# Kernel optimization log

Hardware: AMD Instinct MI355X
Metric: run time of the kernel (lower is better)

The kernel has to match this reference:

```python
import jax, jax.numpy as jnp
import numpy as np

P1 = np.array([[1000.0, 0.0, 128.0, 64000.0],
               [0.0, 1000.0, 128.0, 64000.0],
               [0.0, 0.0, 1.0, 500.0]])
P2 = np.array([[-128.0, 0.0, 1000.0, 64000.0],
               [-128.0, 1000.0, 0.0, 64000.0],
               [-1.0, 0.0, 0.0, 500.0]])


def calculate_fundamental_matrix(P_src, P_dst):
    # l2 = F21 @ x1 : maps a point in P_src onto a line in P_dst
    C1 = -np.linalg.inv(P_src[:3, :3]) @ P_src[:3, 3]
    e = P_dst @ np.append(C1, 1.0)          # epipole of src camera center in dst view
    return np.cross(e, np.eye(3) * -1) @ P_dst @ np.linalg.pinv(P_src)


def setup_inputs() -> dict:
    key = jax.random.key(0)
    view1 = jax.random.normal(key, (8, 4, 256, 256), dtype=jnp.float32)
    F21 = calculate_fundamental_matrix(P1, P2).astype(np.float32)
    return {"view1": view1, "F": jnp.asarray(F21)}


def reference(view1, F):
    """Epipolar image translation: out(x2) = line integral of view1 along the
    epipolar line l1 = F^T @ x2 (bilinear sampling in v, unit steps in u,
    zero outside the image). Matches fume_torch_lib.translate semantics."""
    B, C, H, W = view1.shape
    dt = view1.dtype
    F = F.astype(dt)
    ys = jnp.arange(H, dtype=dt)[:, None]   # (H,1)
    xs = jnp.arange(W, dtype=dt)[None, :]   # (1,W)
    # line coefficients l = F^T @ [x, y, 1], per output pixel -> (H,W)
    a = F[0, 0] * xs + F[1, 0] * ys + F[2, 0]
    b = F[0, 1] * xs + F[1, 1] * ys + F[2, 1]
    c = F[0, 2] * xs + F[1, 2] * ys + F[2, 2]
    n = jnp.sqrt(a * a + b * b) + jnp.asarray(1e-12, dt)
    a, b, c = a / n, b / n, c / n
    ok = (jnp.abs(b) > 1e-6).astype(dt)                 # drop near-vertical lines
    b_safe = jnp.where(jnp.abs(b) > 1e-6, b, jnp.asarray(1.0, dt))

    def step(acc, u):
        uf = u.astype(dt)
        v = -(a * uf + c) / b_safe                      # (H,W) source row per out pixel
        v0 = jnp.floor(v)
        f = v - v0
        i0 = v0.astype(jnp.int32)
        i1 = i0 + 1
        m0 = ((i0 >= 0) & (i0 < H)).astype(dt)
        m1 = ((i1 >= 0) & (i1 < H)).astype(dt)
        col = jax.lax.dynamic_index_in_dim(view1, u, axis=3, keepdims=False)  # (B,C,H)
        s0 = col[:, :, jnp.clip(i0, 0, H - 1)]          # (B,C,H,W)
        s1 = col[:, :, jnp.clip(i1, 0, H - 1)]
        val = (s0 * (1.0 - f) * m0 + s1 * f * m1) * ok
        return acc + val, None

    out, _ = jax.lax.scan(step, jnp.zeros_like(view1), jnp.arange(W))
    return out
```

## Files before the change

### kernel.cpp

```cpp
#include <hip/hip_runtime.h>
#include <cstdint>

constexpr int Hh = 256, Ww = 256, BCc = 32;
constexpr int RBLK = 35;
constexpr int USTRIDE = RBLK * BCc * 8 * 2;

typedef _Float16 half2v  __attribute__((ext_vector_type(2)));
typedef _Float16 half8v  __attribute__((ext_vector_type(8)));
typedef __fp16   fp16x2  __attribute__((ext_vector_type(2)));
typedef float    float4v __attribute__((ext_vector_type(4)));
typedef uint32_t uint4v  __attribute__((ext_vector_type(4)));

static __device__ inline half2v pack2(float a, float b) {
    fp16x2 r = __builtin_amdgcn_cvt_pkrtz(a, b);
    return __builtin_bit_cast(half2v, r);
}

__global__ __launch_bounds__(256) void fume_zero(char* __restrict__ T4) {
    int id = blockIdx.x * 256 + threadIdx.x;
    int u, blk, ch;
    if (id < 257 * 3 * 32) {
        u = id / 96;
        int rem = id - u * 96;
        int bsel = rem >> 5;
        blk = (bsel == 0) ? 0 : (bsel == 1 ? 33 : 34);
        ch = rem & 31;
    } else if (id < 257 * 3 * 32 + 32 * 32) {
        int id2 = id - 257 * 3 * 32;
        u = 256; blk = 1 + (id2 >> 5); ch = id2 & 31;
    } else {
        return;
    }
    uint4v z = {0, 0, 0, 0};
    *(uint4v*)(T4 + (size_t)u * USTRIDE + blk * 512 + ch * 16) = z;
}

__global__ __launch_bounds__(256) void fume_pack(const float* __restrict__ in,
                                                 char* __restrict__ T4) {
    __shared__ float tile[32][65];
    const int t   = threadIdx.x;
    const int bid = blockIdx.x;
    const int chg = bid >> 5;
    const int r0  = ((bid >> 2) & 7) * 32;
    const int u0  = (bid & 3) * 64;

    for (int ci = 0; ci < 8; ++ci) {
        int ch = chg * 8 + ci;
#pragma unroll
        for (int it = 0; it < 8; ++it) {
            int idx = it * 256 + t;
            tile[idx >> 6][idx & 63] =
                in[ch * (Hh * Ww) + (r0 + (idx >> 6)) * Ww + u0 + (idx & 63)];
        }
        __syncthreads();
        int u_l = t >> 2, rs = (t & 3) * 8;
        uint32_t w[4];
#pragma unroll
        for (int j = 0; j < 4; ++j) {
            half2v p = pack2(tile[rs + 2 * j][u_l], tile[rs + 2 * j + 1][u_l]);
            __builtin_memcpy(&w[j], &p, 4);
        }
        int blk = ((r0 + rs) >> 3) + 1;
        uint4v val = {w[0], w[1], w[2], w[3]};
        *(uint4v*)(T4 + (size_t)(u0 + u_l) * USTRIDE + blk * 512 + ch * 16) = val;
        __syncthreads();
    }
}

__global__ __launch_bounds__(256, 8) void fume_mfma(const char* __restrict__ T4,
                                                    const float* __restrict__ Fm,
                                                    float* __restrict__ out) {
    __shared__ float red1[2][16][32];
    __shared__ float red2[2][16][32];
    const int t    = threadIdx.x;
    const int lane = t & 63;
    const int wv   = t >> 6;
    const int uh   = wv & 1;
    const int ly   = wv >> 1;
    const int px   = lane & 15;
    const int quad = lane >> 4;
    const int x0   = ((int)blockIdx.x & 15) * 16;
    const int y    = ((int)blockIdx.x >> 4) * 2 + ly;
    const int x    = x0 + px;

    float xf = (float)x, yf = (float)y;
    float a = Fm[0] * xf + Fm[3] * yf + Fm[6];
    float b = Fm[1] * xf + Fm[4] * yf + Fm[7];
    float c = Fm[2] * xf + Fm[5] * yf + Fm[8];
    float n = sqrtf(a * a + b * b) + 1e-12f;
    a /= n; b /= n; c /= n;

    float alpha, beta_i;
    int u_lo, u_hi;
    if (fabsf(b) > 1e-6f) {
        alpha  = -a / b;
        beta_i = -c / b + 8.f;
        u_lo = 0; u_hi = Ww - 1;
        if (fabsf(alpha) > 1e-12f) {
            float inv = 1.f / alpha;
            float t0 = (7.f - beta_i) * inv;
            float t1 = (264.f - beta_i) * inv;
            int lo = (int)floorf(fminf(t0, t1));
            int hi = (int)ceilf (fmaxf(t0, t1));
            u_lo = lo > 0 ? lo : 0;
            u_hi = hi < (Ww - 1) ? hi : (Ww - 1);
        } else if (beta_i <= 7.f || beta_i >= 264.f) {
            u_lo = 1 << 20; u_hi = -(1 << 20);
        }
    } else {
        alpha = 0.f; beta_i = 3.0e4f;
        u_lo = 1 << 20; u_hi = -(1 << 20);
    }

    float xA = (float)x0, xB = (float)(x0 + 15);
    float aA = Fm[0] * xA + Fm[3] * yf + Fm[6];
    float bA = Fm[1] * xA + Fm[4] * yf + Fm[7];
    float cA = Fm[2] * xA + Fm[5] * yf + Fm[8];
    float aB = Fm[0] * xB + Fm[3] * yf + Fm[6];
    float bB = Fm[1] * xB + Fm[4] * yf + Fm[7];
    float cB = Fm[2] * xB + Fm[5] * yf + Fm[8];
    float alA = -aA / bA, beA = -cA / bA + 8.f;
    float alB = -aB / bB, beB = -cB / bB + 8.f;

    int lo = u_lo, hi = u_hi;
#pragma unroll
    for (int off = 1; off < 64; off <<= 1) {
        int l2 = __shfl_xor(lo, off, 64);
        int h2 = __shfl_xor(hi, off, 64);
        lo = lo < l2 ? lo : l2;
        hi = hi > h2 ? hi : h2;
    }
    lo = __builtin_amdgcn_readfirstlane(lo);
    hi = __builtin_amdgcn_readfirstlane(hi);

    float4v acc0 = {0.f, 0.f, 0.f, 0.f};
    float4v acc1 = {0.f, 0.f, 0.f, 0.f};

    if (lo <= hi) {
        int len = hi - lo + 1;
        int h0  = (((len + 1) >> 1) + 1) & ~1;
        int us, nch;
        if (uh == 0) { us = lo;      nch = h0 >> 1; }
        else {
            int rem = len - h0;
            us = lo + h0;
            nch = rem > 0 ? ((rem + 1) >> 1) : 0;
        }

        float v   = fmaf(alpha, (float)(us + (quad >> 1)), beta_i);
        float a2  = 2.f * alpha;
        float vA0 = fmaf(alA, (float)us, beA);
        float vB0 = fmaf(alB, (float)us, beB);
        float aA2 = 2.f * alA, aB2 = 2.f * alB;
        float lane8 = (float)((quad & 1) * 8);
        const int lane_fix = (quad >> 1) * USTRIDE + (quad & 1) * 512 + px * 16;
        int ubase = us * USTRIDE;

        const half2v one2  = {(_Float16)1.f, (_Float16)1.f};
        const half2v zero2 = {(_Float16)0.f, (_Float16)0.f};

        for (int cc = 0; cc < nch; ++cc) {
            float mn = fminf(fminf(vA0, vA0 + alA), fminf(vB0, vB0 + alB));
            float Mf = floorf(fmaf(mn, 0.125f, -0.125f));
            Mf = fmaxf(0.f, fminf(Mf, 33.f));
            int soff = ubase + ((int)Mf << 9);
            soff = __builtin_amdgcn_readfirstlane(soff);

            uint4v b0 = *(const uint4v*)(T4 + soff + lane_fix);
            uint4v b1 = *(const uint4v*)(T4 + soff + lane_fix + 256);

            float vbl = fmaf(Mf, -8.f, v) - lane8;
            half2v vb2 = pack2(vbl, vbl);
            uint32_t aw[4];
#pragma unroll
            for (int j = 0; j < 4; ++j) {
                half2v cj = {(_Float16)(float)(2 * j),
                             (_Float16)(float)(2 * j + 1)};
                half2v d  = vb2 - cj;
                half2v ad = __builtin_elementwise_abs(d);
                half2v tj = __builtin_elementwise_max(one2 - ad, zero2);
                __builtin_memcpy(&aw[j], &tj, 4);
            }
            half8v A;
            __builtin_memcpy(&A, aw, 16);

            half8v B0 = __builtin_bit_cast(half8v, b0);
            half8v B1 = __builtin_bit_cast(half8v, b1);
            acc0 = __builtin_amdgcn_mfma_f32_16x16x32_f16(A, B0, acc0, 0, 0, 0);
            acc1 = __builtin_amdgcn_mfma_f32_16x16x32_f16(A, B1, acc1, 0, 0, 0);

            v += a2; vA0 += aA2; vB0 += aB2; ubase += 2 * USTRIDE;
        }
    }

    if (uh == 1) {
#pragma unroll
        for (int r = 0; r < 4; ++r) {
            int pm = quad * 4 + r;
            red1[ly][pm][(px + pm) & 31]      = acc0[r];
            red1[ly][pm][(px + 16 + pm) & 31] = acc1[r];
        }
    }
    __syncthreads();
    if (uh == 0) {
#pragma unroll
        for (int r = 0; r < 4; ++r) {
            int pm = quad * 4 + r;
            red2[ly][pm][(px + pm) & 31] =
                acc0[r] + red1[ly][pm][(px + pm) & 31];
            red2[ly][pm][(px + 16 + pm) & 31] =
                acc1[r] + red1[ly][pm][(px + 16 + pm) & 31];
        }
    }
    __syncthreads();
    {
        int ly2 = t >> 7, s = t & 127, pxs = s & 15, cg = s >> 4;
        int yy = ((int)blockIdx.x >> 4) * 2 + ly2;
#pragma unroll
        for (int j = 0; j < 4; ++j) {
            int ch = cg * 4 + j;
            float val = red2[ly2][pxs][(ch + pxs) & 31];
            out[(size_t)ch * (Hh * Ww) + yy * Ww + x0 + pxs] = val;
        }
    }
}

__global__ __launch_bounds__(256) void fume_fallback(const float* __restrict__ src,
                                                     const float* __restrict__ Fm,
                                                     float* __restrict__ out) {
    int g = blockIdx.x * 256 + threadIdx.x;
    int part = g & 3;
    int pix  = g >> 2;
    int x = pix & (Ww - 1);
    int y = pix >> 8;
    int ch0 = part * 8;
    float xf = (float)x, yf = (float)y;
    float a = Fm[0] * xf + Fm[3] * yf + Fm[6];
    float b = Fm[1] * xf + Fm[4] * yf + Fm[7];
    float c = Fm[2] * xf + Fm[5] * yf + Fm[8];
    float n = sqrtf(a * a + b * b) + 1e-12f;
    a /= n; b /= n; c /= n;
    float acc[8];
#pragma unroll
    for (int k = 0; k < 8; ++k) acc[k] = 0.f;
    if (fabsf(b) > 1e-6f) {
        float alpha = -a / b, beta = -c / b;
        for (int u = 0; u < Ww; ++u) {
            float v  = fmaf(alpha, (float)u, beta);
            float rf = floorf(v);
            float f  = v - rf;
            int   ri = (int)rf;
            float w0 = ((unsigned)ri       < (unsigned)Hh) ? (1.f - f) : 0.f;
            float w1 = ((unsigned)(ri + 1) < (unsigned)Hh) ? f         : 0.f;
            int r0 = ri < 0 ? 0 : (ri > Hh - 1 ? Hh - 1 : ri);
            int r1 = ri + 1 < 0 ? 0 : (ri + 1 > Hh - 1 ? Hh - 1 : ri + 1);
#pragma unroll
            for (int k = 0; k < 8; ++k) {
                float s0 = src[(size_t)(ch0 + k) * (Hh * Ww) + r0 * Ww + u];
                float s1 = src[(size_t)(ch0 + k) * (Hh * Ww) + r1 * Ww + u];
                acc[k] = fmaf(w0, s0, fmaf(w1, s1, acc[k]));
            }
        }
    }
#pragma unroll
    for (int k = 0; k < 8; ++k)
        out[(size_t)(ch0 + k) * (Hh * Ww) + pix] = acc[k];
}

extern "C" void kernel_launch(void* const* d_in, const int* in_sizes, int n_in,
                              void* d_out, int out_size, void* d_ws, size_t ws_size,
                              hipStream_t stream) {
    const float* view1 = (const float*)d_in[0];
    const float* Fm    = (const float*)d_in[1];
    float* out = (float*)d_out;

    constexpr size_t t4_bytes = (size_t)257 * USTRIDE;
    if (ws_size >= t4_bytes) {
        char* T4 = (char*)d_ws;
        fume_zero<<<101, 256, 0, stream>>>(T4);
        fume_pack<<<128, 256, 0, stream>>>(view1, T4);
        fume_mfma<<<2048, 256, 0, stream>>>(T4, Fm, out);
    } else {
        fume_fallback<<<(Hh * Ww * 4) / 256, 256, 0, stream>>>(view1, Fm, out);
    }
}
```

Baseline: 113.2 us.

## Fold zero-fill into pack kernel and process u-steps in groups of four

Removes the separate zero-fill launch by giving the pack kernel eight extra blocks that zero the padding planes, and pads the workspace to 264 u-planes. The MFMA inner loop now handles eight u-columns per iteration, issuing four MFMA pairs with one shared row-block offset computed once per group. This cuts per-iteration scalar work and readfirstlane overhead and exposes more independent loads. In exchange it computes padded extra steps that read zeroed planes, and assumes one row block covers the sample span of all eight columns.

```diff
diff --git a/kernel.cpp b/kernel.cpp
--- a/kernel.cpp
+++ b/kernel.cpp
@@ -4,6 +4,7 @@
 constexpr int Hh = 256, Ww = 256, BCc = 32;
 constexpr int RBLK = 35;
 constexpr int USTRIDE = RBLK * BCc * 8 * 2;
+constexpr int UPLANES = 264;
 
 typedef _Float16 half2v  __attribute__((ext_vector_type(2)));
 typedef _Float16 half8v  __attribute__((ext_vector_type(8)));
@@ -16,30 +17,34 @@
     return __builtin_bit_cast(half2v, r);
 }
 
-__global__ __launch_bounds__(256) void fume_zero(char* __restrict__ T4) {
-    int id = blockIdx.x * 256 + threadIdx.x;
-    int u, blk, ch;
-    if (id < 257 * 3 * 32) {
-        u = id / 96;
-        int rem = id - u * 96;
-        int bsel = rem >> 5;
-        blk = (bsel == 0) ? 0 : (bsel == 1 ? 33 : 34);
-        ch = rem & 31;
-    } else if (id < 257 * 3 * 32 + 32 * 32) {
-        int id2 = id - 257 * 3 * 32;
-        u = 256; blk = 1 + (id2 >> 5); ch = id2 & 31;
-    } else {
-        return;
-    }
-    uint4v z = {0, 0, 0, 0};
-    *(uint4v*)(T4 + (size_t)u * USTRIDE + blk * 512 + ch * 16) = z;
-}
-
 __global__ __launch_bounds__(256) void fume_pack(const float* __restrict__ in,
                                                  char* __restrict__ T4) {
-    __shared__ float tile[32][65];
     const int t   = threadIdx.x;
     const int bid = blockIdx.x;
+    if (bid >= 128) {
+        constexpr int NA = UPLANES * 3 * 32;
+        constexpr int NB = 8 * 32 * 32;
+        for (int id = (bid - 128) * 256 + t; id < NA + NB; id += 8 * 256) {
+            int u, blk, ch;
+            if (id < NA) {
+                u = id / 96;
+                int rem = id - u * 96;
+                int bsel = rem >> 5;
+                blk = (bsel == 0) ? 0 : (bsel == 1 ? 33 : 34);
+                ch = rem & 31;
+            } else {
+                int id2 = id - NA;
+                u = 256 + (id2 >> 10);
+                int rem = id2 & 1023;
+                blk = 1 + (rem >> 5);
+                ch = rem & 31;
+            }
+            uint4v z = {0, 0, 0, 0};
+            *(uint4v*)(T4 + (size_t)u * USTRIDE + blk * 512 + ch * 16) = z;
+        }
+        return;
+    }
+    __shared__ float tile[32][65];
     const int chg = bid >> 5;
     const int r0  = ((bid >> 2) & 7) * 32;
     const int u0  = (bid & 3) * 64;
@@ -138,58 +143,61 @@
 
     if (lo <= hi) {
         int len = hi - lo + 1;
-        int h0  = (((len + 1) >> 1) + 1) & ~1;
-        int us, nch;
-        if (uh == 0) { us = lo;      nch = h0 >> 1; }
+        int h0  = (((len + 1) >> 1) + 7) & ~7;
+        int us, ngroups;
+        if (uh == 0) { us = lo; ngroups = h0 >> 3; }
         else {
             int rem = len - h0;
             us = lo + h0;
-            nch = rem > 0 ? ((rem + 1) >> 1) : 0;
+            ngroups = rem > 0 ? ((((rem + 1) >> 1) + 3) >> 2) : 0;
         }
 
         float v   = fmaf(alpha, (float)(us + (quad >> 1)), beta_i);
-        float a2  = 2.f * alpha;
+        float a2  = 2.f * alpha, a8 = 8.f * alpha;
         float vA0 = fmaf(alA, (float)us, beA);
         float vB0 = fmaf(alB, (float)us, beB);
-        float aA2 = 2.f * alA, aB2 = 2.f * alB;
+        float aA8 = 8.f * alA, aB8 = 8.f * alB;
+        float mnA = fminf(7.f * alA, 0.f);
+        float mnB = fminf(7.f * alB, 0.f);
         float lane8 = (float)((quad & 1) * 8);
         const int lane_fix = (quad >> 1) * USTRIDE + (quad & 1) * 512 + px * 16;
-        int ubase = us * USTRIDE;
+        const char* pb = T4 + (size_t)us * USTRIDE + lane_fix;
 
         const half2v one2  = {(_Float16)1.f, (_Float16)1.f};
         const half2v zero2 = {(_Float16)0.f, (_Float16)0.f};
 
-        for (int cc = 0; cc < nch; ++cc) {
-            float mn = fminf(fminf(vA0, vA0 + alA), fminf(vB0, vB0 + alB));
+        for (int g = 0; g < ngroups; ++g) {
+            float mn = fminf(vA0 + mnA, vB0 + mnB);
             float Mf = floorf(fmaf(mn, 0.125f, -0.125f));
             Mf = fmaxf(0.f, fminf(Mf, 33.f));
-            int soff = ubase + ((int)Mf << 9);
-            soff = __builtin_amdgcn_readfirstlane(soff);
-
-            uint4v b0 = *(const uint4v*)(T4 + soff + lane_fix);
-            uint4v b1 = *(const uint4v*)(T4 + soff + lane_fix + 256);
-
-            float vbl = fmaf(Mf, -8.f, v) - lane8;
-            half2v vb2 = pack2(vbl, vbl);
-            uint32_t aw[4];
-#pragma unroll
-            for (int j = 0; j < 4; ++j) {
-                half2v cj = {(_Float16)(float)(2 * j),
-                             (_Float16)(float)(2 * j + 1)};
-                half2v d  = vb2 - cj;
-                half2v ad = __builtin_elementwise_abs(d);
-                half2v tj = __builtin_elementwise_max(one2 - ad, zero2);
-                __builtin_memcpy(&aw[j], &tj, 4);
+            const char* pg = pb + ((int)Mf << 9);
+            float w0 = fmaf(Mf, -8.f, v) - lane8;
+
+#pragma unroll
+            for (int i = 0; i < 4; ++i) {
+                float wi = fmaf((float)i, a2, w0);
+                uint4v b0 = *(const uint4v*)(pg);
+                uint4v b1 = *(const uint4v*)(pg + 256);
+                half2v vb2 = pack2(wi, wi);
+                uint32_t aw[4];
+#pragma unroll
+                for (int j = 0; j < 4; ++j) {
+                    half2v cj = {(_Float16)(float)(2 * j),
+                                 (_Float16)(float)(2 * j + 1)};
+                    half2v d  = vb2 - cj;
+                    half2v ad = __builtin_elementwise_abs(d);
+                    half2v tj = __builtin_elementwise_max(one2 - ad, zero2);
+                    __builtin_memcpy(&aw[j], &tj, 4);
+                }
+                half8v A;
+                __builtin_memcpy(&A, aw, 16);
+                half8v B0 = __builtin_bit_cast(half8v, b0);
+                half8v B1 = __builtin_bit_cast(half8v, b1);
+                acc0 = __builtin_amdgcn_mfma_f32_16x16x32_f16(A, B0, acc0, 0, 0, 0);
+                acc1 = __builtin_amdgcn_mfma_f32_16x16x32_f16(A, B1, acc1, 0, 0, 0);
+                pg += 2 * USTRIDE;
             }
-            half8v A;
-            __builtin_memcpy(&A, aw, 16);
-
-            half8v B0 = __builtin_bit_cast(half8v, b0);
-            half8v B1 = __builtin_bit_cast(half8v, b1);
-            acc0 = __builtin_amdgcn_mfma_f32_16x16x32_f16(A, B0, acc0, 0, 0, 0);
-            acc1 = __builtin_amdgcn_mfma_f32_16x16x32_f16(A, B1, acc1, 0, 0, 0);
-
-            v += a2; vA0 += aA2; vB0 += aB2; ubase += 2 * USTRIDE;
+            v += a8; vA0 += aA8; vB0 += aB8; pb += 8 * USTRIDE;
         }
     }
 
@@ -274,11 +282,10 @@
     const float* Fm    = (const float*)d_in[1];
     float* out = (float*)d_out;
 
-    constexpr size_t t4_bytes = (size_t)257 * USTRIDE;
+    constexpr size_t t4_bytes = (size_t)UPLANES * USTRIDE;
     if (ws_size >= t4_bytes) {
         char* T4 = (char*)d_ws;
-        fume_zero<<<101, 256, 0, stream>>>(T4);
-        fume_pack<<<128, 256, 0, stream>>>(view1, T4);
+        fume_pack<<<136, 256, 0, stream>>>(view1, T4);
         fume_mfma<<<2048, 256, 0, stream>>>(T4, Fm, out);
     } else {
         fume_fallback<<<(Hh * Ww * 4) / 256, 256, 0, stream>>>(view1, Fm, out);
```

After: 104.5 us. -7.6%, faster.
